# Performance work log

Hardware: AMD Instinct MI355X
Metric: run time of the kernel (lower is better)

Reference implementation:

```python
import jax, jax.numpy as jnp
import numpy as np

H = 768
NH = 12
HD = 64
R = 4
SCALING = 8.0 / 4.0  # lora_alpha / r


def setup_inputs() -> dict:
    key = jax.random.key(0)
    ks = jax.random.split(key, 16)
    B, T = 16, 512
    s = 0.02
    x = jax.random.normal(ks[0], (B, T, H), dtype=jnp.float32)
    mask = jax.random.randint(ks[1], (B, T), 0, 2, dtype=jnp.int32)
    return {
        "x": x,
        "mask": mask,
        "Wq": jax.random.normal(ks[2], (H, H), jnp.float32) * s,
        "bq": jnp.zeros((H,), jnp.float32),
        "Aq": jax.random.normal(ks[3], (R, H), jnp.float32) * s,
        "Bq": jax.random.normal(ks[4], (H, R), jnp.float32) * s,
        "Wk": jax.random.normal(ks[5], (H, H), jnp.float32) * s,
        "bk": jnp.zeros((H,), jnp.float32),
        "Wv": jax.random.normal(ks[6], (H, H), jnp.float32) * s,
        "bv": jnp.zeros((H,), jnp.float32),
        "Av": jax.random.normal(ks[7], (R, H), jnp.float32) * s,
        "Bv": jax.random.normal(ks[8], (H, R), jnp.float32) * s,
        "Wo": jax.random.normal(ks[9], (H, H), jnp.float32) * s,
        "bo": jnp.zeros((H,), jnp.float32),
    }


def _lora_linear(x, W, b, A, Bm):
    # base: x @ W^T + b ; lora: (x @ A^T) @ B^T * scaling (dropout inactive at eval)
    return x @ W.T + b + (x @ A.T) @ Bm.T * SCALING


def reference(x, mask, Wq, bq, Aq, Bq, Wk, bk, Wv, bv, Av, Bv, Wo, bo):
    B, T, _ = x.shape
    q = _lora_linear(x, Wq, bq, Aq, Bq).reshape(B, T, NH, HD).transpose(0, 2, 1, 3)
    k = (x @ Wk.T + bk).reshape(B, T, NH, HD).transpose(0, 2, 1, 3)
    v = _lora_linear(x, Wv, bv, Av, Bv).reshape(B, T, NH, HD).transpose(0, 2, 1, 3)
    # [B, NH, T, T]
    scores = jnp.einsum("bhqd,bhkd->bhqk", q, k) / jnp.sqrt(jnp.float32(HD))
    m = (mask == 0)[:, None, None, :]  # mask key positions where mask==0
    scores = jnp.where(m, jnp.float32(-1e9), scores)
    attn = jax.nn.softmax(scores, axis=-1)  # dropout inactive at eval
    out = jnp.einsum("bhqk,bhkd->bhqd", attn, v)
    out = out.transpose(0, 2, 1, 3).reshape(B, T, H)
    return out @ Wo.T + bo
```

## Files before the change

### kernel.cpp

```cpp
#include <hip/hip_runtime.h>
#include <stdint.h>

#define H 768
#define NHEAD 12
#define HDIM 64
#define BATCH 16
#define TSEQ 512
#define BT (BATCH*TSEQ)
#define C3 (3*H)
#define LDQK 1536

typedef __attribute__((ext_vector_type(8))) short short8;
typedef __attribute__((ext_vector_type(4))) float floatx4;
typedef unsigned short u16;

__device__ __forceinline__ u16 f2bf(float f) {
    union { float f; unsigned int u; } v; v.f = f;
    unsigned int u = v.u;
    return (u16)((u + 0x7FFFu + ((u >> 16) & 1u)) >> 16);
}

__device__ __forceinline__ void async_ld16(const void* g, void* l) {
    __builtin_amdgcn_global_load_lds((__attribute__((address_space(1))) void*)g,
                                     (__attribute__((address_space(3))) void*)l,
                                     16, 0, 0);
}

__global__ void prep_weights(const float* __restrict__ Wq, const float* __restrict__ bq,
                             const float* __restrict__ Aq, const float* __restrict__ Bq,
                             const float* __restrict__ Wk, const float* __restrict__ bk,
                             const float* __restrict__ Wv, const float* __restrict__ bv,
                             const float* __restrict__ Av, const float* __restrict__ Bv,
                             const float* __restrict__ Wo,
                             u16* __restrict__ Wall, u16* __restrict__ Wobf,
                             float* __restrict__ bias_all)
{
    const int idx = blockIdx.x * 256 + threadIdx.x;
    const int r = idx / H;
    const int c = idx - r * H;
    if (r < H) {
        float v = Wq[idx] + 2.0f * (Bq[r*4+0]*Aq[c] + Bq[r*4+1]*Aq[H+c] +
                                    Bq[r*4+2]*Aq[2*H+c] + Bq[r*4+3]*Aq[3*H+c]);
        Wall[idx] = f2bf(v);
    } else if (r < 2*H) {
        Wall[idx] = f2bf(Wk[idx - H*H]);
    } else if (r < 3*H) {
        const int rr = r - 2*H;
        float v = Wv[rr*H + c] + 2.0f * (Bv[rr*4+0]*Av[c] + Bv[rr*4+1]*Av[H+c] +
                                         Bv[rr*4+2]*Av[2*H+c] + Bv[rr*4+3]*Av[3*H+c]);
        Wall[idx] = f2bf(v);
    } else {
        Wobf[idx - 3*H*H] = f2bf(Wo[idx - 3*H*H]);
    }
    if (idx < C3) {
        bias_all[idx] = (idx < H) ? bq[idx] : (idx < 2*H ? bk[idx - H] : bv[idx - 2*H]);
    }
}

__global__ void cvt_x_kernel(const float* __restrict__ x, u16* __restrict__ xb)
{
    const int i = (blockIdx.x * 256 + threadIdx.x) * 4;
    const float4 v = *(const float4*)(x + i);
    u16 o[4] = { f2bf(v.x), f2bf(v.y), f2bf(v.z), f2bf(v.w) };
    *(uint2*)(xb + i) = *(const uint2*)o;
}

template<int MODE>
__global__ __launch_bounds__(256)
void gemm_bt(const u16* __restrict__ A, const u16* __restrict__ Bw,
             const float* __restrict__ bias, void* __restrict__ Cout,
             u16* __restrict__ Vout, int K, int ldc)
{
    __shared__ u16 Ablk[128 * 32];
    __shared__ u16 Bblk[128 * 32];
    const int tid  = threadIdx.x;
    const int wave = tid >> 6;
    const int lane = tid & 63;
    const int quad = lane >> 4;
    const int l16  = lane & 15;
    const int m0 = blockIdx.y * 128;
    const int n0 = blockIdx.x * 128;
    const int mw = (wave & 1) * 64;
    const int nw = (wave >> 1) * 64;

    const int srow = lane >> 2;
    const int scol = ((lane & 3) ^ ((lane >> 3) & 3)) * 8;
    const u16* gA = A  + (size_t)(m0 + wave*32 + srow) * K + scol;
    const u16* gB = Bw + (size_t)(n0 + wave*32 + srow) * K + scol;
    u16* lA = Ablk + wave * 32 * 32;
    u16* lB = Bblk + wave * 32 * 32;

    floatx4 acc[4][4] = {};
    const int rsw = ((l16 >> 1) & 3);

    for (int k0 = 0; k0 < K; k0 += 32) {
        __syncthreads();
        async_ld16(gA + k0,          lA);
        async_ld16(gA + k0 + 16*K,   lA + 16*32);
        async_ld16(gB + k0,          lB);
        async_ld16(gB + k0 + 16*K,   lB + 16*32);
        __syncthreads();
        short8 af[4], bfr[4];
        #pragma unroll
        for (int mt = 0; mt < 4; mt++)
            af[mt] = *(const short8*)(Ablk + (mw + mt*16 + l16)*32 + ((quad ^ rsw)*8));
        #pragma unroll
        for (int nt = 0; nt < 4; nt++)
            bfr[nt] = *(const short8*)(Bblk + (nw + nt*16 + l16)*32 + ((quad ^ rsw)*8));
        #pragma unroll
        for (int mt = 0; mt < 4; mt++)
            #pragma unroll
            for (int nt = 0; nt < 4; nt++)
                acc[mt][nt] = __builtin_amdgcn_mfma_f32_16x16x32_bf16(af[mt], bfr[nt], acc[mt][nt], 0, 0, 0);
    }

    if (MODE == 1 && n0 >= LDQK) {
        const int nv = n0 + nw - LDQK;
        const int b  = m0 >> 9;
        #pragma unroll
        for (int nt = 0; nt < 4; nt++) {
            const int n  = nv + nt*16 + l16;
            const int hh = n >> 6, d = n & 63;
            const float bv = bias[LDQK + n];
            u16* vp = Vout + ((size_t)(b*NHEAD + hh) * HDIM + d) * TSEQ;
            #pragma unroll
            for (int mt = 0; mt < 4; mt++) {
                const int t0 = (m0 & 511) + mw + mt*16 + quad*4;
                u16 pack[4];
                #pragma unroll
                for (int r = 0; r < 4; r++) pack[r] = f2bf(acc[mt][nt][r] + bv);
                *(uint2*)(vp + t0) = *(const uint2*)pack;
            }
        }
    } else {
        #pragma unroll
        for (int nt = 0; nt < 4; nt++) {
            const int n = n0 + nw + nt*16 + l16;
            const float bv = bias[n];
            #pragma unroll
            for (int mt = 0; mt < 4; mt++) {
                #pragma unroll
                for (int r = 0; r < 4; r++) {
                    const int m = m0 + mw + mt*16 + quad*4 + r;
                    const float v = acc[mt][nt][r] + bv;
                    if (MODE == 1) ((u16*)Cout)[(size_t)m * ldc + n] = f2bf(v);
                    else           ((float*)Cout)[(size_t)m * ldc + n] = v;
                }
            }
        }
    }
}

#define PSTRIDE 40

__global__ __launch_bounds__(256)
void attn_kernel(const u16* __restrict__ qk, const u16* __restrict__ vt,
                 const int* __restrict__ mask, u16* __restrict__ attn_out)
{
    __shared__ float maskadd[TSEQ];
    __shared__ u16 Kbuf[2][32 * 64];
    __shared__ u16 Vbuf[2][64 * 32];
    __shared__ u16 Pbuf[4][2][16 * PSTRIDE];

    const int qt = blockIdx.x;
    const int bh = blockIdx.y;
    const int b = bh / NHEAD, h = bh - b * NHEAD;
    const int tid  = threadIdx.x;
    const int wave = tid >> 6;
    const int lane = tid & 63;
    const int quad = lane >> 4;
    const int l16  = lane & 15;

    for (int i = tid; i < TSEQ; i += 256)
        maskadd[i] = (mask[b*TSEQ + i] == 0) ? -1e9f : 0.0f;

    const size_t btok = (size_t)b * TSEQ;
    const int q0 = qt * 128 + wave * 32;

    short8 qf[2][2];
    #pragma unroll
    for (int m = 0; m < 2; m++) {
        const u16* qp = qk + (btok + q0 + m*16 + l16) * LDQK + h*HDIM + quad*8;
        qf[m][0] = *(const short8*)qp;
        qf[m][1] = *(const short8*)(qp + 32);
    }

    const u16* kglob = qk + btok * LDQK + H + h*HDIM;
    const u16* vglob = vt + (size_t)bh * HDIM * TSEQ;

    auto stage = [&](int kb, int pp) {
        {
            const int r = lane >> 3;
            const int g = (lane & 7) ^ r;
            async_ld16(kglob + (size_t)(kb + wave*8 + r) * LDQK + g*8,
                       &Kbuf[pp][wave*8*64]);
        }
        {
            const int dr = lane >> 2;
            const int g  = (lane & 3) ^ ((dr >> 1) & 3);
            async_ld16(vglob + (size_t)(wave*16 + dr) * TSEQ + kb + g*8,
                       &Vbuf[pp][wave*16*32]);
        }
    };

    floatx4 o[2][4] = {};
    float lsum[2][4] = {};

    auto compute = [&](int kb, int pp) {
        const u16* Kb_ = Kbuf[pp];
        const u16* Vb_ = Vbuf[pp];
        short8 kf[2][2];
        #pragma unroll
        for (int t = 0; t < 2; t++)
            #pragma unroll
            for (int h2 = 0; h2 < 2; h2++)
                kf[t][h2] = *(const short8*)(Kb_ + (t*16 + l16)*64 + (((h2*4 + quad) ^ (l16 & 7))*8));
        short8 vf[4];
        #pragma unroll
        for (int dt = 0; dt < 4; dt++)
            vf[dt] = *(const short8*)(Vb_ + (dt*16 + l16)*32 + ((quad ^ ((l16 >> 1) & 3))*8));

        floatx4 s[2][2];
        #pragma unroll
        for (int m = 0; m < 2; m++)
            #pragma unroll
            for (int t = 0; t < 2; t++) {
                floatx4 acc = {0.f, 0.f, 0.f, 0.f};
                acc = __builtin_amdgcn_mfma_f32_16x16x32_bf16(qf[m][0], kf[t][0], acc, 0, 0, 0);
                acc = __builtin_amdgcn_mfma_f32_16x16x32_bf16(qf[m][1], kf[t][1], acc, 0, 0, 0);
                s[m][t] = acc;
            }
        const float m0 = maskadd[kb + l16];
        const float m1 = maskadd[kb + 16 + l16];
        #pragma unroll
        for (int m = 0; m < 2; m++) {
            u16* Pw = Pbuf[wave][m];
            #pragma unroll
            for (int r = 0; r < 4; r++) {
                const float p0 = __expf(s[m][0][r] * 0.125f + m0);
                const float p1 = __expf(s[m][1][r] * 0.125f + m1);
                lsum[m][r] += p0 + p1;
                Pw[(quad*4 + r) * PSTRIDE + l16]      = f2bf(p0);
                Pw[(quad*4 + r) * PSTRIDE + 16 + l16] = f2bf(p1);
            }
        }
        #pragma unroll
        for (int m = 0; m < 2; m++) {
            const short8 pa = *(const short8*)(Pbuf[wave][m] + l16 * PSTRIDE + quad*8);
            #pragma unroll
            for (int dt = 0; dt < 4; dt++)
                o[m][dt] = __builtin_amdgcn_mfma_f32_16x16x32_bf16(pa, vf[dt], o[m][dt], 0, 0, 0);
        }
    };

    stage(0, 0);
    for (int it = 0; it < 16; it++) {
        __syncthreads();
        if (it < 15) stage((it + 1) * 32, (it + 1) & 1);
        compute(it * 32, it & 1);
    }

    #pragma unroll
    for (int m = 0; m < 2; m++) {
        float inv[4];
        #pragma unroll
        for (int r = 0; r < 4; r++) {
            float l = lsum[m][r];
            l += __shfl_xor(l, 1);
            l += __shfl_xor(l, 2);
            l += __shfl_xor(l, 4);
            l += __shfl_xor(l, 8);
            inv[r] = 1.0f / l;
        }
        #pragma unroll
        for (int dt = 0; dt < 4; dt++)
            #pragma unroll
            for (int r = 0; r < 4; r++) {
                const int q = q0 + m*16 + quad*4 + r;
                attn_out[(btok + q) * H + h*HDIM + dt*16 + l16] = f2bf(o[m][dt][r] * inv[r]);
            }
    }
}

extern "C" void kernel_launch(void* const* d_in, const int* in_sizes, int n_in,
                              void* d_out, int out_size, void* d_ws, size_t ws_size,
                              hipStream_t stream)
{
    const float* x   = (const float*)d_in[0];
    const int* mask  = (const int*)d_in[1];
    const float* Wq  = (const float*)d_in[2];
    const float* bq  = (const float*)d_in[3];
    const float* Aq  = (const float*)d_in[4];
    const float* Bq  = (const float*)d_in[5];
    const float* Wk  = (const float*)d_in[6];
    const float* bk  = (const float*)d_in[7];
    const float* Wv  = (const float*)d_in[8];
    const float* bv  = (const float*)d_in[9];
    const float* Av  = (const float*)d_in[10];
    const float* Bv  = (const float*)d_in[11];
    const float* Wo  = (const float*)d_in[12];
    const float* bo  = (const float*)d_in[13];

    char* ws = (char*)d_ws;
    u16*   xb      = (u16*)  (ws);
    u16*   Wall    = (u16*)  (ws + 12582912);
    u16*   Wobf    = (u16*)  (ws + 16121856);
    float* biasall = (float*)(ws + 17301504);
    u16*   qk      = (u16*)  (ws + 17310720);
    u16*   vt      = (u16*)  (ws + 42476544);
    u16*   attn_o  = (u16*)  (ws + 55059456);

    prep_weights<<<(4*H*H)/256, 256, 0, stream>>>(Wq, bq, Aq, Bq, Wk, bk, Wv, bv,
                                                  Av, Bv, Wo, Wall, Wobf, biasall);
    cvt_x_kernel<<<(BT*H)/1024, 256, 0, stream>>>(x, xb);
    gemm_bt<1><<<dim3(C3/128, BT/128), 256, 0, stream>>>(xb, Wall, biasall, qk, vt, H, LDQK);
    attn_kernel<<<dim3(TSEQ/128, BATCH*NHEAD), 256, 0, stream>>>(qk, vt, mask, attn_o);
    gemm_bt<0><<<dim3(H/128, BT/128), 256, 0, stream>>>(attn_o, Wobf, bo, d_out, nullptr, H, H);
}
```

Baseline: 223.9 us.

## Double-buffer GEMM LDS tiles and use smaller M tile for output projection

```diff
diff --git a/kernel.cpp b/kernel.cpp
--- a/kernel.cpp
+++ b/kernel.cpp
@@ -65,53 +65,63 @@
     *(uint2*)(xb + i) = *(const uint2*)o;
 }
 
-template<int MODE>
+template<int MODE, int TM>
 __global__ __launch_bounds__(256)
 void gemm_bt(const u16* __restrict__ A, const u16* __restrict__ Bw,
              const float* __restrict__ bias, void* __restrict__ Cout,
              u16* __restrict__ Vout, int K, int ldc)
 {
-    __shared__ u16 Ablk[128 * 32];
-    __shared__ u16 Bblk[128 * 32];
+    constexpr int MT = TM / 32;
+    __shared__ u16 Ablk[2][TM * 32];
+    __shared__ u16 Bblk[2][128 * 32];
     const int tid  = threadIdx.x;
     const int wave = tid >> 6;
     const int lane = tid & 63;
     const int quad = lane >> 4;
     const int l16  = lane & 15;
-    const int m0 = blockIdx.y * 128;
+    const int m0 = blockIdx.y * TM;
     const int n0 = blockIdx.x * 128;
-    const int mw = (wave & 1) * 64;
+    const int mw = (wave & 1) * (TM / 2);
     const int nw = (wave >> 1) * 64;
 
     const int srow = lane >> 2;
-    const int scol = ((lane & 3) ^ ((lane >> 3) & 3)) * 8;
-    const u16* gA = A  + (size_t)(m0 + wave*32 + srow) * K + scol;
+    const int scol = (lane & 3) * 8;
+    const int arow0 = wave * (TM / 4);
+    const u16* gA = A  + (size_t)(m0 + arow0 + srow) * K + scol;
     const u16* gB = Bw + (size_t)(n0 + wave*32 + srow) * K + scol;
-    u16* lA = Ablk + wave * 32 * 32;
-    u16* lB = Bblk + wave * 32 * 32;
-
-    floatx4 acc[4][4] = {};
-    const int rsw = ((l16 >> 1) & 3);
-
-    for (int k0 = 0; k0 < K; k0 += 32) {
-        __syncthreads();
-        async_ld16(gA + k0,          lA);
-        async_ld16(gA + k0 + 16*K,   lA + 16*32);
-        async_ld16(gB + k0,          lB);
-        async_ld16(gB + k0 + 16*K,   lB + 16*32);
-        __syncthreads();
-        short8 af[4], bfr[4];
-        #pragma unroll
-        for (int mt = 0; mt < 4; mt++)
-            af[mt] = *(const short8*)(Ablk + (mw + mt*16 + l16)*32 + ((quad ^ rsw)*8));
+
+    floatx4 acc[MT][4] = {};
+
+    auto stage = [&](int k0, int pp) {
+        u16* lA = Ablk[pp] + arow0 * 32;
+        u16* lB = Bblk[pp] + wave * 32 * 32;
+        async_ld16(gA + k0, lA);
+        if (TM == 128) async_ld16(gA + k0 + 16*K, lA + 16*32);
+        async_ld16(gB + k0, lB);
+        async_ld16(gB + k0 + 16*K, lB + 16*32);
+    };
+
+    auto compute = [&](int pp) {
+        short8 af[MT], bfr[4];
+        #pragma unroll
+        for (int mt = 0; mt < MT; mt++)
+            af[mt] = *(const short8*)(Ablk[pp] + (mw + mt*16 + l16)*32 + quad*8);
         #pragma unroll
         for (int nt = 0; nt < 4; nt++)
-            bfr[nt] = *(const short8*)(Bblk + (nw + nt*16 + l16)*32 + ((quad ^ rsw)*8));
-        #pragma unroll
-        for (int mt = 0; mt < 4; mt++)
+            bfr[nt] = *(const short8*)(Bblk[pp] + (nw + nt*16 + l16)*32 + quad*8);
+        #pragma unroll
+        for (int mt = 0; mt < MT; mt++)
             #pragma unroll
             for (int nt = 0; nt < 4; nt++)
                 acc[mt][nt] = __builtin_amdgcn_mfma_f32_16x16x32_bf16(af[mt], bfr[nt], acc[mt][nt], 0, 0, 0);
+    };
+
+    const int nIter = K >> 5;
+    stage(0, 0);
+    for (int it = 0; it < nIter; it++) {
+        __syncthreads();
+        if (it + 1 < nIter) stage((it + 1) * 32, (it + 1) & 1);
+        compute(it & 1);
     }
 
     if (MODE == 1 && n0 >= LDQK) {
@@ -124,7 +134,7 @@
             const float bv = bias[LDQK + n];
             u16* vp = Vout + ((size_t)(b*NHEAD + hh) * HDIM + d) * TSEQ;
             #pragma unroll
-            for (int mt = 0; mt < 4; mt++) {
+            for (int mt = 0; mt < MT; mt++) {
                 const int t0 = (m0 & 511) + mw + mt*16 + quad*4;
                 u16 pack[4];
                 #pragma unroll
@@ -138,7 +148,7 @@
             const int n = n0 + nw + nt*16 + l16;
             const float bv = bias[n];
             #pragma unroll
-            for (int mt = 0; mt < 4; mt++) {
+            for (int mt = 0; mt < MT; mt++) {
                 #pragma unroll
                 for (int r = 0; r < 4; r++) {
                     const int m = m0 + mw + mt*16 + quad*4 + r;
@@ -313,7 +323,7 @@
     prep_weights<<<(4*H*H)/256, 256, 0, stream>>>(Wq, bq, Aq, Bq, Wk, bk, Wv, bv,
                                                   Av, Bv, Wo, Wall, Wobf, biasall);
     cvt_x_kernel<<<(BT*H)/1024, 256, 0, stream>>>(x, xb);
-    gemm_bt<1><<<dim3(C3/128, BT/128), 256, 0, stream>>>(xb, Wall, biasall, qk, vt, H, LDQK);
+    gemm_bt<1,128><<<dim3(C3/128, BT/128), 256, 0, stream>>>(xb, Wall, biasall, qk, vt, H, LDQK);
     attn_kernel<<<dim3(TSEQ/128, BATCH*NHEAD), 256, 0, stream>>>(qk, vt, mask, attn_o);
-    gemm_bt<0><<<dim3(H/128, BT/128), 256, 0, stream>>>(attn_o, Wobf, bo, d_out, nullptr, H, H);
-}
+    gemm_bt<0,64><<<dim3(H/128, BT/64), 256, 0, stream>>>(attn_o, Wobf, bo, d_out, nullptr, H, H);
+}
```

Measured after the change: 221.3 us. Within noise of the previous version (-1.1%).
